# Kernel tuning notes

Hardware: AMD Instinct MI355X
Metric: run time of the kernel (lower is better)

The kernel has to match this reference:

```python
import jax, jax.numpy as jnp
import numpy as np

B, T, D = 2, 4096, 1024
HQ, HKV, HD = 16, 4, 64   # 16 query heads, 4 KV heads (kv_groups=4), head_dim=64
WIN = 256                 # sliding window radius (left == right == 256)


def setup_inputs() -> dict:
    key = jax.random.key(0)
    ks = jax.random.split(key, 9)
    s = 0.02  # small init scale for stable softmax logits
    return {
        "x": jax.random.normal(ks[0], (B, T, D), jnp.float32),
        "wq": jax.random.normal(ks[1], (D, HQ * HD), jnp.float32) * s,
        "bq": jnp.zeros((HQ * HD,), jnp.float32),
        "wk": jax.random.normal(ks[2], (D, HKV * HD), jnp.float32) * s,
        "bk": jnp.zeros((HKV * HD,), jnp.float32),
        "wv": jax.random.normal(ks[3], (D, HKV * HD), jnp.float32) * s,
        "bv": jnp.zeros((HKV * HD,), jnp.float32),
        "wo": jax.random.normal(ks[4], (HQ * HD, D), jnp.float32) * s,
        "bo": jnp.zeros((D,), jnp.float32),
    }


def _banded_gqa(q, k, v, left, right):
    """Sliding-window GQA attention: query i attends keys in [i-left, i+right].
    Never materializes the full [B,H,T,T] score matrix; uses banded blocks."""
    Bq, Tq, Hq, d = q.shape
    Hkv = k.shape[2]
    G = Hq // Hkv                      # query heads per KV head
    bs = max(left, right)              # block size == window radius; T % bs == 0
    nb = Tq // bs
    # queries: [B, nb, bs, Hkv, G, d]
    qb = q.reshape(Bq, nb, bs, Hkv, G, d)
    # gather 3 neighboring key/value blocks per query block (pad one block each side)
    pad = ((0, 0), (bs, bs), (0, 0), (0, 0))
    idx = jnp.arange(nb)[:, None] * bs + jnp.arange(3 * bs)[None, :]  # into padded seq
    kctx = jnp.pad(k, pad)[:, idx]     # [B, nb, 3bs, Hkv, d]
    vctx = jnp.pad(v, pad)[:, idx]     # [B, nb, 3bs, Hkv, d]
    scale = 1.0 / jnp.sqrt(jnp.asarray(d, q.dtype))
    # banded scores: [B, nb, Hkv, G, bs, 3bs]
    scores = jnp.einsum('bnqhgd,bnkhd->bnhgqk', qb, kctx) * scale
    qpos = jnp.arange(nb)[:, None, None] * bs + jnp.arange(bs)[None, :, None]
    kpos = (jnp.arange(nb)[:, None, None] - 1) * bs + jnp.arange(3 * bs)[None, None, :]
    valid = (kpos >= 0) & (kpos < Tq) & (kpos >= qpos - left) & (kpos <= qpos + right)
    scores = jnp.where(valid[None, :, None, None, :, :], scores, jnp.asarray(-1e30, scores.dtype))
    p = jax.nn.softmax(scores, axis=-1)
    out = jnp.einsum('bnhgqk,bnkhd->bnqhgd', p, vctx)
    return out.reshape(Bq, Tq, Hq, d)


def reference(x, wq, bq, wk, bk, wv, bv, wo, bo):
    q = (x @ wq + bq).reshape(B, T, HQ, HD)
    k = (x @ wk + bk).reshape(B, T, HKV, HD)
    v = (x @ wv + bv).reshape(B, T, HKV, HD)
    y = _banded_gqa(q, k, v, WIN, WIN)       # [B, T, HQ, HD]
    y = y.reshape(B, T, HQ * HD)
    return y @ wo + bo                        # dropout=0.0, deterministic -> identity
```

## Files before the change

### kernel.cpp

```cpp
#include <hip/hip_runtime.h>

typedef unsigned short u16;
typedef u16 u16x4 __attribute__((ext_vector_type(4)));
typedef u16 u16x8 __attribute__((ext_vector_type(8)));
typedef __bf16 bf16x8 __attribute__((ext_vector_type(8)));
typedef float f32x4 __attribute__((ext_vector_type(4)));

#define DEVINL static __device__ __forceinline__

DEVINL u16 f2bf(float f) {
    unsigned u = __builtin_bit_cast(unsigned, f);
    u += 0x7fff + ((u >> 16) & 1);
    return (u16)(u >> 16);
}

DEVINL u16 pbf(float f) {
    unsigned u = __builtin_bit_cast(unsigned, f);
    return (u16)((u + 0x8000) >> 16);
}

DEVINL f32x4 mfma_bf16(u16x8 a, u16x8 b, f32x4 c) {
    return __builtin_amdgcn_mfma_f32_16x16x32_bf16(
        __builtin_bit_cast(bf16x8, a), __builtin_bit_cast(bf16x8, b), c, 0, 0, 0);
}

DEVINL void gload16(const void* g, void* lds) {
    __builtin_amdgcn_global_load_lds(
        (const __attribute__((address_space(1))) void*)g,
        (__attribute__((address_space(3))) void*)lds, 16, 0, 0);
}


__global__ void cvt_x_kernel(const float4* __restrict__ x4, u16x4* __restrict__ o4) {
    int idx = blockIdx.x * 256 + threadIdx.x;
    float4 a = x4[idx];
    u16x4 o;
    o[0] = f2bf(a.x); o[1] = f2bf(a.y); o[2] = f2bf(a.z); o[3] = f2bf(a.w);
    o4[idx] = o;
}

__global__ void fill_bias(const float* __restrict__ bq, const float* __restrict__ bk,
                          const float* __restrict__ bv, float* __restrict__ dst) {
    int i = blockIdx.x * 256 + threadIdx.x;
    if (i < 1024) dst[i] = bq[i];
    else if (i < 1280) dst[i] = bk[i - 1024];
    else if (i < 1536) dst[i] = bv[i - 1280];
}

__global__ void twt_kernel(const float* __restrict__ src, u16* __restrict__ dst,
                           int N, int rowOff) {
    __shared__ float t[64][65];
    int k0 = blockIdx.x * 64, n0 = blockIdx.y * 64;
    int tid = threadIdx.x;
#pragma unroll
    for (int j = 0; j < 16; j++) {
        int idx = j * 256 + tid; int r = idx >> 6, c = idx & 63;
        t[r][c] = src[(size_t)(k0 + r) * N + n0 + c];
    }
    __syncthreads();
#pragma unroll
    for (int j = 0; j < 16; j++) {
        int idx = j * 256 + tid; int r = idx >> 6, c = idx & 63;
        dst[(size_t)(rowOff + n0 + r) * 1024 + k0 + c] = f2bf(t[c][r]);
    }
}

__global__ void tv_kernel(const u16* __restrict__ qkv, u16* __restrict__ vt) {
    __shared__ u16 t[64][68];
    int t0 = blockIdx.x * 64; int h = blockIdx.y; int b = blockIdx.z;
    int tid = threadIdx.x;
#pragma unroll
    for (int j = 0; j < 16; j++) {
        int idx = j * 256 + tid; int r = idx >> 6, c = idx & 63;
        t[r][c] = qkv[(size_t)(b * 4096 + t0 + r) * 1536 + 1280 + h * 64 + c];
    }
    __syncthreads();
#pragma unroll
    for (int j = 0; j < 16; j++) {
        int idx = j * 256 + tid; int r = idx >> 6, c = idx & 63;
        vt[(size_t)((b * 4 + h) * 64 + r) * 4096 + t0 + c] = t[c][r];
    }
}


template <bool F32OUT>
__global__ __launch_bounds__(256, 2) void gemm_bt(
    const u16* __restrict__ A, const u16* __restrict__ Bt, void* __restrict__ Cp,
    const float* __restrict__ bias, int M, int N, int K, int qn, float qscale) {
    __shared__ __align__(16) u16 As[128 * 64];
    __shared__ __align__(16) u16 Bs[128 * 64];
    int tid = threadIdx.x; int l = tid & 63; int w = tid >> 6;
    int m0 = blockIdx.y * 128, n0 = blockIdx.x * 128;
    int wm = (w >> 1) * 64, wn = (w & 1) * 64;
    f32x4 acc[4][4] = {};

    int srow[4], scol[4];
#pragma unroll
    for (int c = 0; c < 4; c++) {
        int b = (w * 4 + c) * 1024 + l * 16;
        int row = b >> 7, inner = b & 127;
        srow[c] = row;
        scol[c] = (inner ^ ((row & 7) << 4)) >> 1;
    }
    int nk = K >> 6;
    for (int kt = 0; kt < nk; ++kt) {
        int kb = kt << 6;
#pragma unroll
        for (int c = 0; c < 4; c++) {
            gload16(A + (size_t)(m0 + srow[c]) * K + kb + scol[c], (char*)As + (w * 4 + c) * 1024);
            gload16(Bt + (size_t)(n0 + srow[c]) * K + kb + scol[c], (char*)Bs + (w * 4 + c) * 1024);
        }
        __syncthreads();
#pragma unroll
        for (int kc = 0; kc < 2; ++kc) {
            int co = (kc * 32 + (l >> 4) * 8) * 2;
            u16x8 af[4], bf[4];
#pragma unroll
            for (int mf = 0; mf < 4; ++mf) {
                int row = wm + mf * 16 + (l & 15);
                af[mf] = *(const u16x8*)((const char*)As + row * 128 + (co ^ ((row & 7) << 4)));
            }
#pragma unroll
            for (int nf = 0; nf < 4; ++nf) {
                int row = wn + nf * 16 + (l & 15);
                bf[nf] = *(const u16x8*)((const char*)Bs + row * 128 + (co ^ ((row & 7) << 4)));
            }
#pragma unroll
            for (int mf = 0; mf < 4; ++mf)
#pragma unroll
                for (int nf = 0; nf < 4; ++nf)
                    acc[mf][nf] = mfma_bf16(af[mf], bf[nf], acc[mf][nf]);
        }
        __syncthreads();
    }
#pragma unroll
    for (int mf = 0; mf < 4; ++mf) {
#pragma unroll
        for (int nf = 0; nf < 4; ++nf) {
            int col = n0 + wn + nf * 16 + (l & 15);
            float bv = bias ? bias[col] : 0.0f;
            float scl = (col < qn) ? qscale : 1.0f;
#pragma unroll
            for (int r = 0; r < 4; r++) {
                int row = m0 + wm + mf * 16 + (l >> 4) * 4 + r;
                float v = (acc[mf][nf][r] + bv) * scl;
                if (F32OUT) ((float*)Cp)[(size_t)row * N + col] = v;
                else        ((u16*)Cp)[(size_t)row * N + col] = f2bf(v);
            }
        }
    }
}


__global__ __launch_bounds__(512, 4) void attn_kernel(
    const u16* __restrict__ qkv, const u16* __restrict__ vt, u16* __restrict__ y) {
    __shared__ __align__(16) u16 Ks[64 * 64];
    __shared__ __align__(16) u16 Vs[64 * 64];
    __shared__ __align__(16) u16 Ps[8][32 * 64];
    int tid = threadIdx.x, l = tid & 63, w = tid >> 6;
    int head = w >> 1, qh = w & 1;
    int qb = ((blockIdx.x & 7) << 3) | (blockIdx.x >> 3);
    int h = blockIdx.y, b = blockIdx.z;
    int qstart = qb * 64;
    size_t rowbase = (size_t)b * 4096;
    int hq = h * 4 + head;

    u16x8 qf_[2][2];
#pragma unroll
    for (int qf = 0; qf < 2; ++qf)
#pragma unroll
        for (int kc = 0; kc < 2; ++kc)
            qf_[qf][kc] = *(const u16x8*)(qkv + (rowbase + qstart + qh * 32 + qf * 16 + (l & 15)) * 1536
                                          + hq * 64 + kc * 32 + (l >> 4) * 8);

    f32x4 o[2][4] = {};
    float mrow[2], srow_[2];
#pragma unroll
    for (int i = 0; i < 2; i++) { mrow[i] = -__builtin_inff(); srow_[i] = 0.f; }

    const u16* kbase_ptr = qkv + 1024 + h * 64;
    const u16* vbase_ptr = vt + (size_t)((b * 4 + h) * 64) * 4096;

    int sb_ = w * 1024 + l * 16;
    int g_row = sb_ >> 7, g_inner = sb_ & 127;
    int g_col = (g_inner ^ ((g_row & 7) << 4)) >> 1;

#pragma unroll
    for (int kstart = qstart - 256; kstart <= qstart + 256; kstart += 64) {
        if (kstart < 0 || kstart >= 4096) continue;
        gload16(kbase_ptr + (rowbase + kstart + g_row) * 1536 + g_col, (char*)Ks + w * 1024);
        gload16(vbase_ptr + (size_t)g_row * 4096 + kstart + g_col, (char*)Vs + w * 1024);
        __syncthreads();

        f32x4 st[4][2] = {};
#pragma unroll
        for (int kc = 0; kc < 2; ++kc) {
            int co = (kc * 32 + (l >> 4) * 8) * 2;
            u16x8 kf_[4];
#pragma unroll
            for (int kf = 0; kf < 4; ++kf) {
                int row = kf * 16 + (l & 15);
                kf_[kf] = *(const u16x8*)((const char*)Ks + row * 128 + (co ^ ((row & 7) << 4)));
            }
#pragma unroll
            for (int kf = 0; kf < 4; ++kf)
#pragma unroll
                for (int qf = 0; qf < 2; ++qf)
                    st[kf][qf] = mfma_bf16(kf_[kf], qf_[qf][kc], st[kf][qf]);
        }

        bool mlo = (kstart == qstart - 256);
        bool mhi = (kstart == qstart + 256);

#pragma unroll
        for (int qf = 0; qf < 2; ++qf) {
            int qoff = qh * 32 + qf * 16 + (l & 15);
            float pmax = -1e30f;
            float sv[4][4];
#pragma unroll
            for (int kf = 0; kf < 4; ++kf)
#pragma unroll
                for (int r = 0; r < 4; r++) {
                    int koff = kf * 16 + (l >> 4) * 4 + r;
                    float v = st[kf][qf][r];
                    if (mlo && koff < qoff) v = -1e30f;
                    if (mhi && koff > qoff) v = -1e30f;
                    sv[kf][r] = v;
                    pmax = fmaxf(pmax, v);
                }
            pmax = fmaxf(pmax, __shfl_xor(pmax, 16));
            pmax = fmaxf(pmax, __shfl_xor(pmax, 32));

            bool resc = !__all(pmax - mrow[qf] <= 8.0f);
            float newm = resc ? fmaxf(mrow[qf], pmax) : mrow[qf];
            float psum = 0.f;
#pragma unroll
            for (int kf = 0; kf < 4; ++kf) {
                u16x4 pk;
#pragma unroll
                for (int r = 0; r < 4; r++) {
                    float e = __builtin_amdgcn_exp2f(sv[kf][r] - newm);
                    psum += e;
                    pk[r] = pbf(e);
                }
                int row = qf * 16 + (l & 15);
                int keyc = kf * 16 + (l >> 4) * 4;
                *(u16x4*)((char*)Ps[w] + ((row * 128 + keyc * 2) ^ ((row & 7) << 4))) = pk;
            }
            psum += __shfl_xor(psum, 16);
            psum += __shfl_xor(psum, 32);
            if (resc) {
                float fs = __builtin_amdgcn_exp2f(mrow[qf] - newm);
                srow_[qf] = srow_[qf] * fs + psum;
                mrow[qf] = newm;
#pragma unroll
                for (int r = 0; r < 4; r++) {
                    float fb = __shfl(fs, (l >> 4) * 4 + r);
#pragma unroll
                    for (int nf = 0; nf < 4; ++nf) o[qf][nf][r] *= fb;
                }
            } else {
                srow_[qf] += psum;
            }
        }

#pragma unroll
        for (int kc = 0; kc < 2; ++kc) {
            int co = (kc * 32 + (l >> 4) * 8) * 2;
            u16x8 vb[4];
#pragma unroll
            for (int nf = 0; nf < 4; ++nf) {
                int row = nf * 16 + (l & 15);
                vb[nf] = *(const u16x8*)((const char*)Vs + row * 128 + (co ^ ((row & 7) << 4)));
            }
#pragma unroll
            for (int mf = 0; mf < 2; ++mf) {
                int row = mf * 16 + (l & 15);
                u16x8 pa = *(const u16x8*)((const char*)Ps[w] + ((row * 128 + co) ^ ((row & 7) << 4)));
#pragma unroll
                for (int nf = 0; nf < 4; ++nf)
                    o[mf][nf] = mfma_bf16(pa, vb[nf], o[mf][nf]);
            }
        }
        __syncthreads();
    }

#pragma unroll
    for (int mf = 0; mf < 2; ++mf) {
        float inv = 1.0f / srow_[mf];
#pragma unroll
        for (int r = 0; r < 4; r++) {
            float sb = __shfl(inv, (l >> 4) * 4 + r);
            int row = qstart + qh * 32 + mf * 16 + (l >> 4) * 4 + r;
#pragma unroll
            for (int nf = 0; nf < 4; ++nf) {
                int col = hq * 64 + nf * 16 + (l & 15);
                y[(rowbase + row) * 1024 + col] = f2bf(o[mf][nf][r] * sb);
            }
        }
    }
}


extern "C" void kernel_launch(void* const* d_in, const int* in_sizes, int n_in,
                              void* d_out, int out_size, void* d_ws, size_t ws_size,
                              hipStream_t stream) {
    const float* x  = (const float*)d_in[0];
    const float* wq = (const float*)d_in[1];
    const float* bq = (const float*)d_in[2];
    const float* wk = (const float*)d_in[3];
    const float* bk = (const float*)d_in[4];
    const float* wv = (const float*)d_in[5];
    const float* bv = (const float*)d_in[6];
    const float* wo = (const float*)d_in[7];
    const float* bo = (const float*)d_in[8];
    float* out = (float*)d_out;

    char* p = (char*)d_ws;
    u16* xb     = (u16*)p;   p += (size_t)8192 * 1024 * 2;
    u16* wqkvt  = (u16*)p;   p += (size_t)1536 * 1024 * 2;
    u16* wot    = (u16*)p;   p += (size_t)1024 * 1024 * 2;
    float* bqkv = (float*)p; p += 8192;
    u16* qkvb   = (u16*)p;   p += (size_t)8192 * 1536 * 2;
    u16* vtb    = (u16*)p;   p += (size_t)512 * 4096 * 2;
    u16* yb     = (u16*)p;

    cvt_x_kernel<<<8192, 256, 0, stream>>>((const float4*)x, (u16x4*)xb);
    fill_bias<<<6, 256, 0, stream>>>(bq, bk, bv, bqkv);
    twt_kernel<<<dim3(16, 16), 256, 0, stream>>>(wq, wqkvt, 1024, 0);
    twt_kernel<<<dim3(16, 4),  256, 0, stream>>>(wk, wqkvt, 256, 1024);
    twt_kernel<<<dim3(16, 4),  256, 0, stream>>>(wv, wqkvt, 256, 1280);
    twt_kernel<<<dim3(16, 16), 256, 0, stream>>>(wo, wot, 1024, 0);

    gemm_bt<false><<<dim3(12, 64), 256, 0, stream>>>(xb, wqkvt, qkvb, bqkv,
                                                     8192, 1536, 1024, 1024, 0.18033688f);
    tv_kernel<<<dim3(64, 4, 2), 256, 0, stream>>>(qkvb, vtb);
    attn_kernel<<<dim3(64, 4, 2), 512, 0, stream>>>(qkvb, vtb, yb);
    gemm_bt<true><<<dim3(8, 64), 256, 0, stream>>>(yb, wot, out, bo,
                                                   8192, 1024, 1024, 0, 1.0f);
}
```

Measured before the change: 127.8 us.

## Split attention blocks across head pairs and remap GEMM workgroups per XCD

The attention kernel now launches twice as many blocks. Each block handles two query heads of a KV group instead of four, and each wave processes 16 query rows instead of 32. This halves per-wave registers and the P tile, and the occupancy hint rises to 8. The aim is more parallelism and better latency hiding, at the cost of loading each K/V tile twice. Separately, the GEMM remaps workgroup IDs so consecutive tiles land on the same XCD for L2 locality.

```diff
diff --git a/kernel.cpp b/kernel.cpp
--- a/kernel.cpp
+++ b/kernel.cpp
@@ -90,7 +90,14 @@
     __shared__ __align__(16) u16 As[128 * 64];
     __shared__ __align__(16) u16 Bs[128 * 64];
     int tid = threadIdx.x; int l = tid & 63; int w = tid >> 6;
-    int m0 = blockIdx.y * 128, n0 = blockIdx.x * 128;
+
+    int nwg = gridDim.x * gridDim.y;
+    int lin = blockIdx.y * gridDim.x + blockIdx.x;
+    int q_ = nwg >> 3, r_ = nwg & 7;
+    int xcd = lin & 7, i_ = lin >> 3;
+    int wgid = (xcd < r_ ? xcd * (q_ + 1) : r_ * (q_ + 1) + (xcd - r_) * q_) + i_;
+    int m0 = (wgid / gridDim.x) * 128, n0 = (wgid % gridDim.x) * 128;
+
     int wm = (w >> 1) * 64, wn = (w & 1) * 64;
     f32x4 acc[4][4] = {};
 
@@ -152,31 +159,27 @@
 }
 
 
-__global__ __launch_bounds__(512, 4) void attn_kernel(
+__global__ __launch_bounds__(512, 8) void attn_kernel(
     const u16* __restrict__ qkv, const u16* __restrict__ vt, u16* __restrict__ y) {
     __shared__ __align__(16) u16 Ks[64 * 64];
     __shared__ __align__(16) u16 Vs[64 * 64];
-    __shared__ __align__(16) u16 Ps[8][32 * 64];
+    __shared__ __align__(16) u16 Ps[8][16 * 64];
     int tid = threadIdx.x, l = tid & 63, w = tid >> 6;
-    int head = w >> 1, qh = w & 1;
     int qb = ((blockIdx.x & 7) << 3) | (blockIdx.x >> 3);
-    int h = blockIdx.y, b = blockIdx.z;
+    int h = blockIdx.y >> 1, hp = blockIdx.y & 1, b = blockIdx.z;
     int qstart = qb * 64;
     size_t rowbase = (size_t)b * 4096;
-    int hq = h * 4 + head;
-
-    u16x8 qf_[2][2];
-#pragma unroll
-    for (int qf = 0; qf < 2; ++qf)
-#pragma unroll
-        for (int kc = 0; kc < 2; ++kc)
-            qf_[qf][kc] = *(const u16x8*)(qkv + (rowbase + qstart + qh * 32 + qf * 16 + (l & 15)) * 1536
-                                          + hq * 64 + kc * 32 + (l >> 4) * 8);
-
-    f32x4 o[2][4] = {};
-    float mrow[2], srow_[2];
-#pragma unroll
-    for (int i = 0; i < 2; i++) { mrow[i] = -__builtin_inff(); srow_[i] = 0.f; }
+    int hq = h * 4 + hp * 2 + (w >> 2);
+    int qrow0 = (w & 3) * 16;
+
+    u16x8 qf_[2];
+#pragma unroll
+    for (int kc = 0; kc < 2; ++kc)
+        qf_[kc] = *(const u16x8*)(qkv + (rowbase + qstart + qrow0 + (l & 15)) * 1536
+                                  + hq * 64 + kc * 32 + (l >> 4) * 8);
+
+    f32x4 o[4] = {};
+    float mrow = -__builtin_inff(), srow_ = 0.f;
 
     const u16* kbase_ptr = qkv + 1024 + h * 64;
     const u16* vbase_ptr = vt + (size_t)((b * 4 + h) * 64) * 4096;
@@ -192,111 +195,94 @@
         gload16(vbase_ptr + (size_t)g_row * 4096 + kstart + g_col, (char*)Vs + w * 1024);
         __syncthreads();
 
-        f32x4 st[4][2] = {};
+        f32x4 st[4] = {};
 #pragma unroll
         for (int kc = 0; kc < 2; ++kc) {
             int co = (kc * 32 + (l >> 4) * 8) * 2;
-            u16x8 kf_[4];
 #pragma unroll
             for (int kf = 0; kf < 4; ++kf) {
                 int row = kf * 16 + (l & 15);
-                kf_[kf] = *(const u16x8*)((const char*)Ks + row * 128 + (co ^ ((row & 7) << 4)));
-            }
-#pragma unroll
-            for (int kf = 0; kf < 4; ++kf)
-#pragma unroll
-                for (int qf = 0; qf < 2; ++qf)
-                    st[kf][qf] = mfma_bf16(kf_[kf], qf_[qf][kc], st[kf][qf]);
+                u16x8 kfr = *(const u16x8*)((const char*)Ks + row * 128 + (co ^ ((row & 7) << 4)));
+                st[kf] = mfma_bf16(kfr, qf_[kc], st[kf]);
+            }
         }
 
         bool mlo = (kstart == qstart - 256);
         bool mhi = (kstart == qstart + 256);
 
-#pragma unroll
-        for (int qf = 0; qf < 2; ++qf) {
-            int qoff = qh * 32 + qf * 16 + (l & 15);
-            float pmax = -1e30f;
-            float sv[4][4];
-#pragma unroll
-            for (int kf = 0; kf < 4; ++kf)
-#pragma unroll
-                for (int r = 0; r < 4; r++) {
-                    int koff = kf * 16 + (l >> 4) * 4 + r;
-                    float v = st[kf][qf][r];
-                    if (mlo && koff < qoff) v = -1e30f;
-                    if (mhi && koff > qoff) v = -1e30f;
-                    sv[kf][r] = v;
-                    pmax = fmaxf(pmax, v);
-                }
-            pmax = fmaxf(pmax, __shfl_xor(pmax, 16));
-            pmax = fmaxf(pmax, __shfl_xor(pmax, 32));
-
-            bool resc = !__all(pmax - mrow[qf] <= 8.0f);
-            float newm = resc ? fmaxf(mrow[qf], pmax) : mrow[qf];
-            float psum = 0.f;
-#pragma unroll
-            for (int kf = 0; kf < 4; ++kf) {
-                u16x4 pk;
-#pragma unroll
-                for (int r = 0; r < 4; r++) {
-                    float e = __builtin_amdgcn_exp2f(sv[kf][r] - newm);
-                    psum += e;
-                    pk[r] = pbf(e);
-                }
-                int row = qf * 16 + (l & 15);
-                int keyc = kf * 16 + (l >> 4) * 4;
-                *(u16x4*)((char*)Ps[w] + ((row * 128 + keyc * 2) ^ ((row & 7) << 4))) = pk;
-            }
-            psum += __shfl_xor(psum, 16);
-            psum += __shfl_xor(psum, 32);
-            if (resc) {
-                float fs = __builtin_amdgcn_exp2f(mrow[qf] - newm);
-                srow_[qf] = srow_[qf] * fs + psum;
-                mrow[qf] = newm;
-#pragma unroll
-                for (int r = 0; r < 4; r++) {
-                    float fb = __shfl(fs, (l >> 4) * 4 + r);
-#pragma unroll
-                    for (int nf = 0; nf < 4; ++nf) o[qf][nf][r] *= fb;
-                }
-            } else {
-                srow_[qf] += psum;
-            }
+        int qoff = qrow0 + (l & 15);
+        float pmax = -1e30f;
+        float sv[4][4];
+#pragma unroll
+        for (int kf = 0; kf < 4; ++kf)
+#pragma unroll
+            for (int r = 0; r < 4; r++) {
+                int koff = kf * 16 + (l >> 4) * 4 + r;
+                float v = st[kf][r];
+                if (mlo && koff < qoff) v = -1e30f;
+                if (mhi && koff > qoff) v = -1e30f;
+                sv[kf][r] = v;
+                pmax = fmaxf(pmax, v);
+            }
+        pmax = fmaxf(pmax, __shfl_xor(pmax, 16));
+        pmax = fmaxf(pmax, __shfl_xor(pmax, 32));
+
+        bool resc = !__all(pmax - mrow <= 8.0f);
+        float newm = resc ? fmaxf(mrow, pmax) : mrow;
+        float psum = 0.f;
+#pragma unroll
+        for (int kf = 0; kf < 4; ++kf) {
+            u16x4 pk;
+#pragma unroll
+            for (int r = 0; r < 4; r++) {
+                float e = __builtin_amdgcn_exp2f(sv[kf][r] - newm);
+                psum += e;
+                pk[r] = pbf(e);
+            }
+            int row = l & 15;
+            int keyc = kf * 16 + (l >> 4) * 4;
+            *(u16x4*)((char*)Ps[w] + ((row * 128 + keyc * 2) ^ ((row & 7) << 4))) = pk;
+        }
+        psum += __shfl_xor(psum, 16);
+        psum += __shfl_xor(psum, 32);
+        if (resc) {
+            float fs = __builtin_amdgcn_exp2f(mrow - newm);
+            srow_ = srow_ * fs + psum;
+            mrow = newm;
+#pragma unroll
+            for (int r = 0; r < 4; r++) {
+                float fb = __shfl(fs, (l >> 4) * 4 + r);
+#pragma unroll
+                for (int nf = 0; nf < 4; ++nf) o[nf][r] *= fb;
+            }
+        } else {
+            srow_ += psum;
         }
 
 #pragma unroll
         for (int kc = 0; kc < 2; ++kc) {
             int co = (kc * 32 + (l >> 4) * 8) * 2;
-            u16x8 vb[4];
+            int prow = l & 15;
+            u16x8 pa = *(const u16x8*)((const char*)Ps[w] + ((prow * 128 + co) ^ ((prow & 7) << 4)));
 #pragma unroll
             for (int nf = 0; nf < 4; ++nf) {
                 int row = nf * 16 + (l & 15);
-                vb[nf] = *(const u16x8*)((const char*)Vs + row * 128 + (co ^ ((row & 7) << 4)));
-            }
-#pragma unroll
-            for (int mf = 0; mf < 2; ++mf) {
-                int row = mf * 16 + (l & 15);
-                u16x8 pa = *(const u16x8*)((const char*)Ps[w] + ((row * 128 + co) ^ ((row & 7) << 4)));
-#pragma unroll
-                for (int nf = 0; nf < 4; ++nf)
-                    o[mf][nf] = mfma_bf16(pa, vb[nf], o[mf][nf]);
+                u16x8 vb = *(const u16x8*)((const char*)Vs + row * 128 + (co ^ ((row & 7) << 4)));
+                o[nf] = mfma_bf16(pa, vb, o[nf]);
             }
         }
         __syncthreads();
     }
 
-#pragma unroll
-    for (int mf = 0; mf < 2; ++mf) {
-        float inv = 1.0f / srow_[mf];
-#pragma unroll
-        for (int r = 0; r < 4; r++) {
-            float sb = __shfl(inv, (l >> 4) * 4 + r);
-            int row = qstart + qh * 32 + mf * 16 + (l >> 4) * 4 + r;
-#pragma unroll
-            for (int nf = 0; nf < 4; ++nf) {
-                int col = hq * 64 + nf * 16 + (l & 15);
-                y[(rowbase + row) * 1024 + col] = f2bf(o[mf][nf][r] * sb);
-            }
+    float inv = 1.0f / srow_;
+#pragma unroll
+    for (int r = 0; r < 4; r++) {
+        float sb = __shfl(inv, (l >> 4) * 4 + r);
+        int row = qstart + qrow0 + (l >> 4) * 4 + r;
+#pragma unroll
+        for (int nf = 0; nf < 4; ++nf) {
+            int col = hq * 64 + nf * 16 + (l & 15);
+            y[(rowbase + row) * 1024 + col] = f2bf(o[nf][r] * sb);
         }
     }
 }
@@ -335,7 +321,7 @@
     gemm_bt<false><<<dim3(12, 64), 256, 0, stream>>>(xb, wqkvt, qkvb, bqkv,
                                                      8192, 1536, 1024, 1024, 0.18033688f);
     tv_kernel<<<dim3(64, 4, 2), 256, 0, stream>>>(qkvb, vtb);
-    attn_kernel<<<dim3(64, 4, 2), 512, 0, stream>>>(qkvb, vtb, yb);
+    attn_kernel<<<dim3(64, 8, 2), 512, 0, stream>>>(qkvb, vtb, yb);
     gemm_bt<true><<<dim3(8, 64), 256, 0, stream>>>(yb, wot, out, bo,
                                                    8192, 1024, 1024, 0, 1.0f);
 }
```

New measurement: 130.3 us. Within noise of the previous version (+2.0%).
